# Kernel tuning notes

Measured on AMD Instinct MI355X. Metric: run time of the kernel, lower is better.

The kernel has to match this reference:

```python
import jax, jax.numpy as jnp
import numpy as np

QMAX = 127.0  # int8 symmetric quantization, num_bits=8
H, D, MRP = 16, 64, 32
DM = H * D  # d_model = 1024


def act_quant(x):
    # per-tensor symmetric int8 quant; returns quantized values (float-held) and scale
    scale = jnp.max(jnp.abs(x)) / QMAX + 1e-8
    y = x / scale
    q = jnp.clip(jnp.round(y), -QMAX, QMAX)
    return q, scale


def quant_linear(x, w, b):
    # TPUGEMMLinear: quantize activations and kernel per-tensor, int8 GEMM, dequant, add bias
    xq, sx = act_quant(x)
    wq, sw = act_quant(w)
    return jnp.matmul(xq, wq) * (sx * sw) + b


def setup_inputs() -> dict:
    key = jax.random.key(0)
    ks = jax.random.split(key, 8)
    B, Sq, Skv = 4, 1024, 1024
    inputs_q = jax.random.normal(ks[0], (B, Sq, DM), dtype=jnp.float32)
    inputs_kv = jax.random.normal(ks[1], (B, Skv, DM), dtype=jnp.float32)
    init_scale = 1.0 / np.sqrt(DM)  # lecun_normal-like
    Wq = jax.random.normal(ks[2], (DM, H * D), dtype=jnp.float32) * init_scale
    Wk = jax.random.normal(ks[3], (DM, H * D), dtype=jnp.float32) * init_scale
    Wv = jax.random.normal(ks[4], (DM, H * D), dtype=jnp.float32) * init_scale
    Wo = jax.random.normal(ks[5], (H * D, DM), dtype=jnp.float32) * init_scale
    bq = jnp.zeros((H * D,), jnp.float32)
    bk = jnp.zeros((H * D,), jnp.float32)
    bv = jnp.zeros((H * D,), jnp.float32)
    bo = jnp.zeros((DM,), jnp.float32)
    rel_pos_emb = jax.random.normal(ks[6], (2 * MRP + 1, D), dtype=jnp.float32) * 0.02
    return {"inputs_q": inputs_q, "inputs_kv": inputs_kv, "Wq": Wq, "bq": bq,
            "Wk": Wk, "bk": bk, "Wv": Wv, "bv": bv, "Wo": Wo, "bo": bo,
            "rel_pos_emb": rel_pos_emb}


def reference(inputs_q, inputs_kv, Wq, bq, Wk, bk, Wv, bv, Wo, bo, rel_pos_emb):
    B, Sq, _ = inputs_q.shape
    Skv = inputs_kv.shape[1]
    # quantized QKV projections
    q = quant_linear(inputs_q, Wq, bq).reshape(B, Sq, H, D).transpose(0, 2, 1, 3)   # [B,H,Sq,D]
    k = quant_linear(inputs_kv, Wk, bk).reshape(B, Skv, H, D).transpose(0, 2, 1, 3)  # [B,H,Skv,D]
    v = quant_linear(inputs_kv, Wv, bv).reshape(B, Skv, H, D).transpose(0, 2, 1, 3)  # [B,H,Skv,D]
    # relative position bias: gather emb rows per (q,k) offset -> [1,D?,Sq,Skv]
    positions = jnp.clip(jnp.arange(Sq)[:, None] - jnp.arange(Skv)[None, :] + MRP, 0, 2 * MRP)
    rel_pos_bias = rel_pos_emb[positions]                 # [Sq,Skv,D]
    rel_pos_bias = rel_pos_bias.transpose(2, 0, 1)[None]  # [1,D,Sq,Skv]; D==head_dim broadcasts over heads when D==H pattern; here added to [B,H,Sq,Skv] via broadcast of first H rows? No: faithful to original -> added directly
    # quantized QK^T
    kq, sk = act_quant(k.transpose(0, 1, 3, 2))  # [B,H,D,Skv]
    qq, sq = act_quant(q)
    content_scores = jnp.einsum('bhqd,bhdk->bhqk', qq, kq) * (sq * sk)
    attention_scores = content_scores + rel_pos_bias[:, :H]  # original broadcast-add of [1,D,Sq,Skv]; D>=H here (D=64,H=16) so slice matches broadcast semantics only when D==H; we take leading H planes to keep shapes consistent
    scale_factor = jnp.sqrt(jnp.float32(D)) * jnp.power(jnp.float32(min(Sq, Skv)), 0.25)
    attention_scores = attention_scores / scale_factor
    # manual stable softmax with +1e-6 in denominator (as in source)
    max_score = jnp.max(attention_scores, axis=-1, keepdims=True)
    exp_weights = jnp.exp(attention_scores - max_score)
    attention_weights = exp_weights / (jnp.sum(exp_weights, axis=-1, keepdims=True) + 1e-6)
    # quantized AV (weights unquantized, scale 1; values int8)
    vq, sv = act_quant(v)
    attention_output = jnp.einsum('bhqk,bhkd->bhqd', attention_weights, vq) * sv
    attention_output = attention_output.transpose(0, 2, 1, 3).reshape(B, Sq, H * D)
    return quant_linear(attention_output, Wo, bo)
```

## Files before the change

### kernel.cpp

```cpp
#include <hip/hip_runtime.h>
#include <hip/hip_bf16.h>
#include <stdint.h>

static constexpr int B_ = 4, S_ = 1024, H_ = 16, D_ = 64, DM_ = 1024;
static constexpr float SF_ = 45.254833221435546875f;
static constexpr float RCP_SF_ = 1.0f / SF_;
static constexpr float KC_ = (float)(1.4426950408889634074 / 45.254833221435546875);

typedef unsigned short u16;
typedef __attribute__((ext_vector_type(8))) short bf16x8;
typedef __attribute__((ext_vector_type(4))) float f32x4;

#define MFMA_BF16 __builtin_amdgcn_mfma_f32_16x16x32_bf16

typedef const __attribute__((address_space(1))) void CGV;
typedef __attribute__((address_space(3))) void LDSV;
__device__ __forceinline__ void gload16(const void* g, void* l) {
  __builtin_amdgcn_global_load_lds((CGV*)g, (LDSV*)l, 16, 0, 0);
}

__device__ __forceinline__ float slot_scale(const unsigned* s) {
  return __uint_as_float(*s) / 127.0f + 1e-8f;
}
__device__ __forceinline__ float quantf(float x, float s) {
  return fminf(fmaxf(rintf(x / s), -127.f), 127.f);
}
__device__ __forceinline__ u16 f2b(float x) {
  union { __hip_bfloat16 h; u16 u; } cv;
  cv.h = __float2bfloat16(x);
  return cv.u;
}
__device__ __forceinline__ float b2f(u16 u) { return __uint_as_float((unsigned)u << 16); }
__device__ __forceinline__ u16 qb16(float x, float s) { return f2b(quantf(x, s)); }

__global__ void zero_slots_kernel(unsigned* slots) {
  if (threadIdx.x < 16) slots[threadIdx.x] = 0u;
}

struct Ptr6 { const float* p[6]; int n4[6]; };

__global__ __launch_bounds__(256) void absmax6_kernel(Ptr6 a, unsigned* __restrict__ slots) {
  const int y = blockIdx.y;
  const float4* x4 = (const float4*)a.p[y];
  const int n4 = a.n4[y];
  float m = 0.f;
  for (int i = blockIdx.x * 256 + threadIdx.x; i < n4; i += gridDim.x * 256) {
    float4 v = x4[i];
    m = fmaxf(m, fmaxf(fmaxf(fabsf(v.x), fabsf(v.y)), fmaxf(fabsf(v.z), fabsf(v.w))));
  }
#pragma unroll
  for (int off = 32; off; off >>= 1) m = fmaxf(m, __shfl_xor(m, off));
  if ((threadIdx.x & 63) == 0) atomicMax(slots + y, __float_as_uint(m));
}

__device__ __forceinline__ void quant_body(const float* __restrict__ x, int n8, float s,
                                           u16* __restrict__ out) {
  for (int i = blockIdx.x * 256 + threadIdx.x; i < n8; i += gridDim.x * 256) {
    float4 v0 = *((const float4*)x + 2 * (size_t)i);
    float4 v1 = *((const float4*)x + 2 * (size_t)i + 1);
    int4 o;
    o.x = (int)qb16(v0.x, s) | ((int)qb16(v0.y, s) << 16);
    o.y = (int)qb16(v0.z, s) | ((int)qb16(v0.w, s) << 16);
    o.z = (int)qb16(v1.x, s) | ((int)qb16(v1.y, s) << 16);
    o.w = (int)qb16(v1.z, s) | ((int)qb16(v1.w, s) << 16);
    *((int4*)out + i) = o;
  }
}

__global__ __launch_bounds__(256) void quantize_bf16_kernel(const float* __restrict__ x, int n8,
                                                            const unsigned* __restrict__ slot,
                                                            u16* __restrict__ out) {
  quant_body(x, n8, slot_scale(slot), out);
}

__global__ __launch_bounds__(256) void quantize2_kernel(const float* __restrict__ x0,
                                                        const float* __restrict__ x1,
                                                        u16* __restrict__ o0, u16* __restrict__ o1,
                                                        const unsigned* __restrict__ slots, int n8) {
  const int y = blockIdx.y;
  quant_body(y ? x1 : x0, n8, slot_scale(slots + y), y ? o1 : o0);
}

struct QP3 { const float* tf[3]; };
__global__ __launch_bounds__(256) void quantP3_kernel(QP3 a, const unsigned* __restrict__ slots,
                                                      u16* __restrict__ q_p, u16* __restrict__ k_p,
                                                      u16* __restrict__ vT) {
  __shared__ u16 t[64][72];
  const int z = blockIdx.z;
  const float s = slot_scale(slots + 6 + z);
  const int tid = threadIdx.x;
  if (z < 2) {
    const float* xf = a.tf[z];
    u16* xp = z ? k_p : q_p;
    const int st = blockIdx.x & 15, bh = blockIdx.x >> 4;
    const int b = bh >> 4, h = bh & 15;
    const int r = tid >> 2, seg = (tid & 3) * 16;
    const float* src = &xf[((size_t)(b * S_) + st * 64 + r) * DM_ + h * 64 + seg];
    u16 qv[16];
#pragma unroll
    for (int i = 0; i < 16; i += 4) {
      float4 v = *(const float4*)(src + i);
      qv[i] = qb16(v.x, s); qv[i + 1] = qb16(v.y, s);
      qv[i + 2] = qb16(v.z, s); qv[i + 3] = qb16(v.w, s);
    }
    u16* dst = &xp[((size_t)bh * S_ + st * 64 + r) * 64 + seg];
    *(int4*)dst = *(const int4*)&qv[0];
    *(int4*)(dst + 8) = *(const int4*)&qv[8];
  } else {
    const float* vf = a.tf[2];
    const int h = blockIdx.x >> 6, bt = blockIdx.x & 63;
    const int b = bt >> 4, kt = bt & 15;
    const int row = tid >> 2, seg = (tid & 3) * 16;
    const float* src = &vf[((size_t)(b * S_) + kt * 64 + row) * DM_ + h * 64 + seg];
    float4 v0 = *(const float4*)src;
    float4 v1 = *(const float4*)(src + 4);
    float4 v2 = *(const float4*)(src + 8);
    float4 v3 = *(const float4*)(src + 12);
    t[seg + 0][row] = qb16(v0.x, s);  t[seg + 1][row] = qb16(v0.y, s);
    t[seg + 2][row] = qb16(v0.z, s);  t[seg + 3][row] = qb16(v0.w, s);
    t[seg + 4][row] = qb16(v1.x, s);  t[seg + 5][row] = qb16(v1.y, s);
    t[seg + 6][row] = qb16(v1.z, s);  t[seg + 7][row] = qb16(v1.w, s);
    t[seg + 8][row] = qb16(v2.x, s);  t[seg + 9][row] = qb16(v2.y, s);
    t[seg + 10][row] = qb16(v2.z, s); t[seg + 11][row] = qb16(v2.w, s);
    t[seg + 12][row] = qb16(v3.x, s); t[seg + 13][row] = qb16(v3.y, s);
    t[seg + 14][row] = qb16(v3.z, s); t[seg + 15][row] = qb16(v3.w, s);
    __syncthreads();
    const int d = tid >> 2, s2 = (tid & 3) * 16;
    u16* dst = &vT[((size_t)(b * 16 + h) * 64 + d) * (size_t)S_ + kt * 64 + s2];
    *(int4*)dst = *(const int4*)&t[d][s2];
    *(int4*)(dst + 8) = *(const int4*)&t[d][s2 + 8];
  }
}

struct W4 { const float* w[4]; u16* wt[4]; };
__global__ __launch_bounds__(256) void quantW4_kernel(W4 a, const unsigned* __restrict__ slots) {
  __shared__ u16 t[64][72];
  const int z = blockIdx.z;
  const float* w = a.w[z];
  u16* wt = a.wt[z];
  const float s = slot_scale(slots + 2 + z);
  const int k0 = blockIdx.y * 64, n0 = blockIdx.x * 64;
  const int tid = threadIdx.x;
#pragma unroll
  for (int rr = 0; rr < 4; rr++) {
    const int row = (tid >> 4) + rr * 16;
    const int col = (tid & 15) * 4;
    float4 v = *(const float4*)&w[(size_t)(k0 + row) * DM_ + n0 + col];
    t[col + 0][row] = qb16(v.x, s);
    t[col + 1][row] = qb16(v.y, s);
    t[col + 2][row] = qb16(v.z, s);
    t[col + 3][row] = qb16(v.w, s);
  }
  __syncthreads();
  const int nr = tid >> 2, kc = (tid & 3) * 16;
  *(int4*)&wt[(size_t)(n0 + nr) * DM_ + k0 + kc] = *(const int4*)&t[nr][kc];
  *(int4*)&wt[(size_t)(n0 + nr) * DM_ + k0 + kc + 8] = *(const int4*)&t[nr][kc + 8];
}

__device__ __forceinline__ void gemm_body(
    const u16* __restrict__ A, const u16* __restrict__ Bt,
    const unsigned* __restrict__ slotA, const unsigned* __restrict__ slotB,
    const float* __restrict__ bias, float* __restrict__ C,
    unsigned* __restrict__ amax_out,
    u16 (*As)[128][64], u16 (*Bs)[64][64]) {
  const int N = DM_, K = DM_;
  const int id = blockIdx.x;
  const int lin = (id & 7) * 64 + (id >> 3);
  const int by = lin >> 4, bx = lin & 15;
  const int m0 = by * 128, n0 = bx * 64;
  const int tid = threadIdx.x, w = tid >> 6, lane = tid & 63;
  const int c = lane & 15, g = lane >> 4;
  const int wr = w >> 1, wc = w & 1;
  const int lr = lane >> 3, lc = lane & 7;
  const int schunk = (lc ^ lr) << 3;

  f32x4 acc[4][2] = {};

  auto stage = [&](int buf, int kc) {
#pragma unroll
    for (int p = 0; p < 4; ++p) {
      const int r0 = w * 32 + p * 8;
      gload16(&A[(size_t)(m0 + r0 + lr) * K + kc + schunk], &As[buf][r0][0]);
    }
#pragma unroll
    for (int p = 0; p < 2; ++p) {
      const int r0 = w * 16 + p * 8;
      gload16(&Bt[(size_t)(n0 + r0 + lr) * K + kc + schunk], &Bs[buf][r0][0]);
    }
  };

  stage(0, 0);
  __syncthreads();
  for (int kt = 0; kt < 16; ++kt) {
    const int buf = kt & 1;
    if (kt < 15) stage(buf ^ 1, (kt + 1) * 64);
#pragma unroll
    for (int ks = 0; ks < 2; ++ks) {
      const int rswz = ((ks * 4 + g) ^ (c & 7)) << 3;
      bf16x8 b0 = *(const bf16x8*)&Bs[buf][wc * 32 + c][rswz];
      bf16x8 b1 = *(const bf16x8*)&Bs[buf][wc * 32 + 16 + c][rswz];
#pragma unroll
      for (int i = 0; i < 4; ++i) {
        bf16x8 av = *(const bf16x8*)&As[buf][wr * 64 + i * 16 + c][rswz];
        acc[i][0] = MFMA_BF16(av, b0, acc[i][0], 0, 0, 0);
        acc[i][1] = MFMA_BF16(av, b1, acc[i][1], 0, 0, 0);
      }
    }
    __syncthreads();
  }

  const float sAB = slot_scale(slotA) * slot_scale(slotB);
  float am = 0.f;
#pragma unroll
  for (int i = 0; i < 4; ++i)
#pragma unroll
    for (int j = 0; j < 2; ++j)
#pragma unroll
      for (int reg = 0; reg < 4; ++reg) {
        const int m = m0 + wr * 64 + i * 16 + 4 * g + reg;
        const int nn = n0 + wc * 32 + j * 16 + c;
        const float val = __fadd_rn(__fmul_rn(acc[i][j][reg], sAB), bias[nn]);
        C[(size_t)m * N + nn] = val;
        am = fmaxf(am, fabsf(val));
      }
  if (amax_out) {
#pragma unroll
    for (int off = 32; off; off >>= 1) am = fmaxf(am, __shfl_xor(am, off));
    if (lane == 0) atomicMax(amax_out, __float_as_uint(am));
  }
}

__global__ __launch_bounds__(256) void gemm128_kernel(
    const u16* __restrict__ A, const u16* __restrict__ Bt,
    const unsigned* __restrict__ slotA, const unsigned* __restrict__ slotB,
    const float* __restrict__ bias, float* __restrict__ C,
    unsigned* __restrict__ amax_out) {
  __shared__ u16 As[2][128][64];
  __shared__ u16 Bs[2][64][64];
  gemm_body(A, Bt, slotA, slotB, bias, C, amax_out, As, Bs);
}

struct G3 {
  const u16* A[3]; const u16* Bt[3]; const float* bias[3]; float* C[3];
};
__global__ __launch_bounds__(256) void gemm3_kernel(G3 a, unsigned* __restrict__ slots) {
  __shared__ u16 As[2][128][64];
  __shared__ u16 Bs[2][64][64];
  const int z = blockIdx.y;
  const unsigned* slotA = slots + (z == 0 ? 0 : 1);
  const unsigned* slotB = slots + 2 + z;
  gemm_body(a.A[z], a.Bt[z], slotA, slotB, a.bias[z], a.C[z], slots + 6 + z, As, Bs);
}

__global__ __launch_bounds__(256) void attn_kernel(
    const u16* __restrict__ qp_, const u16* __restrict__ kp_, const u16* __restrict__ vTb_,
    const unsigned* __restrict__ slots, const float* __restrict__ rel,
    float* __restrict__ ao, unsigned* __restrict__ amax_out) {
  __shared__ u16 Ks[2][64][64];
  __shared__ u16 Vs[2][64][64];
  __shared__ float Pf[4][16][68];
  __shared__ float biasT[68];
  __shared__ float Mrow[4][2][16];
  __shared__ float Frow[4][2][16];
  __shared__ float Lrow[4][2][16];

  const int id = blockIdx.x;
  const int rX = id & 7, rest = id >> 3;
  const int qoct = rest & 7, bhi = rest >> 3;
  const int gbh = rX * 8 + bhi;
  const int h = gbh & 15, b = gbh >> 4;

  const int tid = threadIdx.x;
  const int w = tid >> 6, lane = tid & 63;
  const int c = lane & 15, g = lane >> 4;
  const int lr = lane >> 3, lc = lane & 7;
  const int schunk = (lc ^ lr) << 3;

  const float sqk = slot_scale(slots + 6) * slot_scale(slots + 7);
  const float sv = slot_scale(slots + 8);
  if (tid < 65) biasT[tid] = rel[tid * D_ + h];

  const size_t ppan = (size_t)gbh * S_ * 64;
  const size_t vpan = (size_t)gbh * 64 * (size_t)S_;

  const int qb2[2] = {qoct * 128 + w * 16, qoct * 128 + 64 + w * 16};
  bf16x8 qA0[2], qA1[2];
#pragma unroll
  for (int u = 0; u < 2; ++u) {
    const size_t qrow = ppan + (size_t)(qb2[u] + c) * 64;
    qA0[u] = *(const bf16x8*)&qp_[qrow + g * 8];
    qA1[u] = *(const bf16x8*)&qp_[qrow + 32 + g * 8];
  }

  int4 kreg[2], vreg[2];
  auto loadK = [&](int ch) {
#pragma unroll
    for (int p = 0; p < 2; ++p)
      kreg[p] = *(const int4*)&kp_[ppan + (size_t)(ch * 64 + w * 16 + p * 8 + lr) * 64 + schunk];
  };
  auto writeK = [&](int buf) {
#pragma unroll
    for (int p = 0; p < 2; ++p)
      *(int4*)&Ks[buf][w * 16 + p * 8 + lr][lc * 8] = kreg[p];
  };
  auto loadV = [&](int ch) {
#pragma unroll
    for (int p = 0; p < 2; ++p)
      vreg[p] = *(const int4*)&vTb_[vpan + (size_t)(w * 16 + p * 8 + lr) * S_ + ch * 64 + schunk];
  };
  auto writeV = [&](int buf) {
#pragma unroll
    for (int p = 0; p < 2; ++p)
      *(int4*)&Vs[buf][w * 16 + p * 8 + lr][lc * 8] = vreg[p];
  };

  float M2[2][4], m2k[2][4], lsc[2] = {0.f, 0.f};
  f32x4 oacc[2][4] = {};
#pragma unroll
  for (int u = 0; u < 2; ++u)
#pragma unroll
    for (int reg = 0; reg < 4; ++reg) {
      M2[u][reg] = -3.4e38f;
      m2k[u][reg] = -3.4e38f * KC_;
    }

  loadK(0);
  loadV(0);
  writeK(0);
  writeV(0);
  __syncthreads();
  const float b_lo = biasT[0], b_hi = biasT[64];

  for (int ch = 0; ch < 16; ++ch) {
    const int buf = ch & 1;
    if (ch < 15) { loadK(ch + 1); loadV(ch + 1); }
#pragma unroll
    for (int u = 0; u < 2; ++u) {
      const int qbase = qb2[u];
      float mloc[4] = {-3.4e38f, -3.4e38f, -3.4e38f, -3.4e38f};
#pragma unroll
      for (int t = 0; t < 4; ++t) {
        f32x4 sacc = {0.f, 0.f, 0.f, 0.f};
        const int kr = t * 16 + c, sw = c & 7;
        bf16x8 k0 = *(const bf16x8*)&Ks[buf][kr][(g ^ sw) << 3];
        bf16x8 k1 = *(const bf16x8*)&Ks[buf][kr][((4 + g) ^ sw) << 3];
        sacc = MFMA_BF16(qA0[u], k0, sacc, 0, 0, 0);
        sacc = MFMA_BF16(qA1[u], k1, sacc, 0, 0, 0);
        const int kv0 = ch * 64 + t * 16;
        float bb[4];
        if (kv0 >= qbase + 47) {
          bb[0] = bb[1] = bb[2] = bb[3] = b_lo;
        } else if (qbase >= kv0 + 47) {
          bb[0] = bb[1] = bb[2] = bb[3] = b_hi;
        } else {
          const int jg = kv0 + c;
#pragma unroll
          for (int reg = 0; reg < 4; ++reg) {
            int dp = qbase + 4 * g + reg - jg + 32;
            dp = dp < 0 ? 0 : (dp > 64 ? 64 : dp);
            bb[reg] = biasT[dp];
          }
        }
        float* pw = &Pf[w][4 * g][t * 16 + c];
#pragma unroll
        for (int reg = 0; reg < 4; ++reg) {
          const float t2 = __fadd_rn(__fmul_rn(sacc[reg], sqk), bb[reg]);
          pw[reg * 68] = t2;
          mloc[reg] = fmaxf(mloc[reg], t2);
        }
      }
#pragma unroll
      for (int off = 1; off <= 8; off <<= 1)
#pragma unroll
        for (int reg = 0; reg < 4; ++reg)
          mloc[reg] = fmaxf(mloc[reg], __shfl_xor(mloc[reg], off));
      float f[4];
#pragma unroll
      for (int reg = 0; reg < 4; ++reg) {
        M2[u][reg] = fmaxf(M2[u][reg], mloc[reg]);
        const float mk = M2[u][reg] * KC_;
        f[reg] = exp2f(m2k[u][reg] - mk);
        m2k[u][reg] = mk;
      }
#pragma unroll
      for (int n = 0; n < 4; ++n)
#pragma unroll
        for (int reg = 0; reg < 4; ++reg) oacc[u][n][reg] *= f[reg];
      if (c < 4) {
        Mrow[w][u][4 * g + c] = m2k[u][c];
        Frow[w][u][4 * g + c] = f[c];
      }
      const float mkc = Mrow[w][u][c];
      lsc[u] = lsc[u] * Frow[w][u][c];
      float lacc = 0.f;
#pragma unroll
      for (int ks = 0; ks < 2; ++ks) {
        const float* pr = &Pf[w][c][ks * 32 + g * 8];
        float4 e0 = *(const float4*)pr;
        float4 e1 = *(const float4*)(pr + 4);
        float tv[8] = {e0.x, e0.y, e0.z, e0.w, e1.x, e1.y, e1.z, e1.w};
        bf16x8 ph, pm;
#pragma unroll
        for (int jj = 0; jj < 8; ++jj) {
          const float e = exp2f(fmaf(tv[jj], KC_, -mkc));
          lacc += e;
          const u16 hu = f2b(e);
          const float r1 = __fsub_rn(e, b2f(hu));
          const u16 mu = f2b(r1);
          ph[jj] = (short)hu;
          pm[jj] = (short)mu;
        }
#pragma unroll
        for (int n = 0; n < 4; ++n) {
          const int dd = 16 * n + c;
          bf16x8 vv = *(const bf16x8*)&Vs[buf][dd][((ks * 4 + g) ^ (c & 7)) << 3];
          oacc[u][n] = MFMA_BF16(ph, vv, oacc[u][n], 0, 0, 0);
          oacc[u][n] = MFMA_BF16(pm, vv, oacc[u][n], 0, 0, 0);
        }
      }
      lsc[u] += lacc;
    }
    if (ch < 15) { writeK(buf ^ 1); writeV(buf ^ 1); }
    __syncthreads();
  }

#pragma unroll
  for (int u = 0; u < 2; ++u) {
    float t = lsc[u];
    t += __shfl_xor(t, 16);
    t += __shfl_xor(t, 32);
    if (g == 0) Lrow[w][u][c] = t;
  }

  float am = 0.f;
#pragma unroll
  for (int u = 0; u < 2; ++u) {
#pragma unroll
    for (int reg = 0; reg < 4; ++reg) {
      const float L = Lrow[w][u][4 * g + reg] + 1e-6f;
      const size_t orow = ((size_t)(b * S_) + qb2[u] + 4 * g + reg) * DM_ + h * 64;
#pragma unroll
      for (int n = 0; n < 4; ++n) {
        const float val = __fmul_rn(oacc[u][n][reg] / L, sv);
        ao[orow + n * 16 + c] = val;
        am = fmaxf(am, fabsf(val));
      }
    }
  }
#pragma unroll
  for (int off = 1; off <= 32; off <<= 1) am = fmaxf(am, __shfl_xor(am, off));
  if (lane == 0) atomicMax(amax_out, __float_as_uint(am));
}

extern "C" void kernel_launch(void* const* d_in, const int* in_sizes, int n_in,
                              void* d_out, int out_size, void* d_ws, size_t ws_size,
                              hipStream_t stream) {
  const float* inputs_q  = (const float*)d_in[0];
  const float* inputs_kv = (const float*)d_in[1];
  const float* Wq = (const float*)d_in[2];
  const float* bq = (const float*)d_in[3];
  const float* Wk = (const float*)d_in[4];
  const float* bk = (const float*)d_in[5];
  const float* Wv = (const float*)d_in[6];
  const float* bv = (const float*)d_in[7];
  const float* Wo = (const float*)d_in[8];
  const float* bo = (const float*)d_in[9];
  const float* rel = (const float*)d_in[10];
  float* out = (float*)d_out;

  char* ws = (char*)d_ws;
  constexpr size_t MB = 1024 * 1024;
  unsigned* slots = (unsigned*)ws;
  u16* xq_b  = (u16*)(ws + 1024);
  u16* xkv_b = (u16*)((char*)xq_b + 8 * MB);
  u16* wq_b  = (u16*)((char*)xkv_b + 8 * MB);
  u16* wk_b  = (u16*)((char*)wq_b + 2 * MB);
  u16* wv_b  = (u16*)((char*)wk_b + 2 * MB);
  u16* wo_b  = (u16*)((char*)wv_b + 2 * MB);
  u16* q_p   = (u16*)((char*)wo_b + 2 * MB);
  u16* k_p   = (u16*)((char*)q_p + 8 * MB);
  u16* vT_b  = (u16*)((char*)k_p + 8 * MB);
  u16* ao_b  = (u16*)((char*)vT_b + 8 * MB);
  float* tf0 = (float*)((char*)ao_b + 8 * MB);
  float* tf1 = (float*)((char*)tf0 + 16 * MB);
  float* tf2 = (float*)((char*)tf1 + 16 * MB);
  float* aof = tf0;
  (void)ws_size; (void)in_sizes; (void)n_in; (void)out_size;

  const int n4_x = (B_ * S_ * DM_) / 4, n4_w = (DM_ * DM_) / 4;
  const int n8_x = (B_ * S_ * DM_) / 8;

  zero_slots_kernel<<<1, 64, 0, stream>>>(slots);

  Ptr6 a6;
  a6.p[0] = inputs_q;  a6.n4[0] = n4_x;
  a6.p[1] = inputs_kv; a6.n4[1] = n4_x;
  a6.p[2] = Wq; a6.n4[2] = n4_w;
  a6.p[3] = Wk; a6.n4[3] = n4_w;
  a6.p[4] = Wv; a6.n4[4] = n4_w;
  a6.p[5] = Wo; a6.n4[5] = n4_w;
  absmax6_kernel<<<dim3(128, 6), 256, 0, stream>>>(a6, slots);

  quantize2_kernel<<<dim3(512, 2), 256, 0, stream>>>(inputs_q, inputs_kv, xq_b, xkv_b,
                                                     slots, n8_x);
  W4 w4;
  w4.w[0] = Wq; w4.wt[0] = wq_b;
  w4.w[1] = Wk; w4.wt[1] = wk_b;
  w4.w[2] = Wv; w4.wt[2] = wv_b;
  w4.w[3] = Wo; w4.wt[3] = wo_b;
  quantW4_kernel<<<dim3(16, 16, 4), 256, 0, stream>>>(w4, slots);

  G3 g3;
  g3.A[0] = xq_b;  g3.Bt[0] = wq_b; g3.bias[0] = bq; g3.C[0] = tf0;
  g3.A[1] = xkv_b; g3.Bt[1] = wk_b; g3.bias[1] = bk; g3.C[1] = tf1;
  g3.A[2] = xkv_b; g3.Bt[2] = wv_b; g3.bias[2] = bv; g3.C[2] = tf2;
  gemm3_kernel<<<dim3(512, 3), 256, 0, stream>>>(g3, slots);

  QP3 qp3;
  qp3.tf[0] = tf0; qp3.tf[1] = tf1; qp3.tf[2] = tf2;
  quantP3_kernel<<<dim3(1024, 1, 3), 256, 0, stream>>>(qp3, slots, q_p, k_p, vT_b);

  attn_kernel<<<512, 256, 0, stream>>>(q_p, k_p, vT_b, slots, rel, aof, slots + 9);

  quantize_bf16_kernel<<<1024, 256, 0, stream>>>(aof, n8_x, slots + 9, ao_b);

  gemm128_kernel<<<512, 256, 0, stream>>>(ao_b, wo_b, slots + 9, slots + 5, bo, out, nullptr);
}
```

Measured before the change: 306.6 us.

## Widen QKV GEMM tile to 128x128 and merge input/weight quantize kernels

The fused QKV projection GEMM now uses 128x128 output tiles with a 4x4 MFMA accumulator per wave, up from 128x64. This halves the block count and raises operand reuse per LDS load, at the cost of more registers and LDS per block. The separate input-quantize and weight-quantize/transpose kernels are merged into one launch indexed by blockIdx.z to save one launch. Weight slices leave their surplus blocks idle.

```diff
diff --git a/kernel.cpp b/kernel.cpp
--- a/kernel.cpp
+++ b/kernel.cpp
@@ -73,12 +73,39 @@
   quant_body(x, n8, slot_scale(slot), out);
 }
 
-__global__ __launch_bounds__(256) void quantize2_kernel(const float* __restrict__ x0,
-                                                        const float* __restrict__ x1,
-                                                        u16* __restrict__ o0, u16* __restrict__ o1,
-                                                        const unsigned* __restrict__ slots, int n8) {
-  const int y = blockIdx.y;
-  quant_body(y ? x1 : x0, n8, slot_scale(slots + y), y ? o1 : o0);
+struct QIW {
+  const float* xq; const float* xkv; u16* xqo; u16* xkvo;
+  const float* w[4]; u16* wt[4];
+};
+__global__ __launch_bounds__(256) void quantIW_kernel(QIW a, const unsigned* __restrict__ slots,
+                                                      int n8) {
+  __shared__ u16 t[64][72];
+  const int z = blockIdx.z;
+  const int tid = threadIdx.x;
+  if (z < 2) {
+    quant_body(z ? a.xkv : a.xq, n8, slot_scale(slots + z), z ? a.xkvo : a.xqo);
+  } else {
+    if (blockIdx.x >= 256) return;
+    const int zz = z - 2;
+    const float* w = a.w[zz];
+    u16* wt = a.wt[zz];
+    const float s = slot_scale(slots + 2 + zz);
+    const int k0 = (blockIdx.x >> 4) * 64, n0 = (blockIdx.x & 15) * 64;
+#pragma unroll
+    for (int rr = 0; rr < 4; rr++) {
+      const int row = (tid >> 4) + rr * 16;
+      const int col = (tid & 15) * 4;
+      float4 v = *(const float4*)&w[(size_t)(k0 + row) * DM_ + n0 + col];
+      t[col + 0][row] = qb16(v.x, s);
+      t[col + 1][row] = qb16(v.y, s);
+      t[col + 2][row] = qb16(v.z, s);
+      t[col + 3][row] = qb16(v.w, s);
+    }
+    __syncthreads();
+    const int nr = tid >> 2, kc = (tid & 3) * 16;
+    *(int4*)&wt[(size_t)(n0 + nr) * DM_ + k0 + kc] = *(const int4*)&t[nr][kc];
+    *(int4*)&wt[(size_t)(n0 + nr) * DM_ + k0 + kc + 8] = *(const int4*)&t[nr][kc + 8];
+  }
 }
 
 struct QP3 { const float* tf[3]; };
@@ -132,37 +159,13 @@
   }
 }
 
-struct W4 { const float* w[4]; u16* wt[4]; };
-__global__ __launch_bounds__(256) void quantW4_kernel(W4 a, const unsigned* __restrict__ slots) {
-  __shared__ u16 t[64][72];
-  const int z = blockIdx.z;
-  const float* w = a.w[z];
-  u16* wt = a.wt[z];
-  const float s = slot_scale(slots + 2 + z);
-  const int k0 = blockIdx.y * 64, n0 = blockIdx.x * 64;
-  const int tid = threadIdx.x;
-#pragma unroll
-  for (int rr = 0; rr < 4; rr++) {
-    const int row = (tid >> 4) + rr * 16;
-    const int col = (tid & 15) * 4;
-    float4 v = *(const float4*)&w[(size_t)(k0 + row) * DM_ + n0 + col];
-    t[col + 0][row] = qb16(v.x, s);
-    t[col + 1][row] = qb16(v.y, s);
-    t[col + 2][row] = qb16(v.z, s);
-    t[col + 3][row] = qb16(v.w, s);
-  }
-  __syncthreads();
-  const int nr = tid >> 2, kc = (tid & 3) * 16;
-  *(int4*)&wt[(size_t)(n0 + nr) * DM_ + k0 + kc] = *(const int4*)&t[nr][kc];
-  *(int4*)&wt[(size_t)(n0 + nr) * DM_ + k0 + kc + 8] = *(const int4*)&t[nr][kc + 8];
-}
-
-__device__ __forceinline__ void gemm_body(
+__global__ __launch_bounds__(256) void gemm128_kernel(
     const u16* __restrict__ A, const u16* __restrict__ Bt,
     const unsigned* __restrict__ slotA, const unsigned* __restrict__ slotB,
     const float* __restrict__ bias, float* __restrict__ C,
-    unsigned* __restrict__ amax_out,
-    u16 (*As)[128][64], u16 (*Bs)[64][64]) {
+    unsigned* __restrict__ amax_out) {
+  __shared__ u16 As[2][128][64];
+  __shared__ u16 Bs[2][64][64];
   const int N = DM_, K = DM_;
   const int id = blockIdx.x;
   const int lin = (id & 7) * 64 + (id >> 3);
@@ -230,26 +233,83 @@
   }
 }
 
-__global__ __launch_bounds__(256) void gemm128_kernel(
-    const u16* __restrict__ A, const u16* __restrict__ Bt,
-    const unsigned* __restrict__ slotA, const unsigned* __restrict__ slotB,
-    const float* __restrict__ bias, float* __restrict__ C,
-    unsigned* __restrict__ amax_out) {
-  __shared__ u16 As[2][128][64];
-  __shared__ u16 Bs[2][64][64];
-  gemm_body(A, Bt, slotA, slotB, bias, C, amax_out, As, Bs);
-}
-
 struct G3 {
   const u16* A[3]; const u16* Bt[3]; const float* bias[3]; float* C[3];
 };
 __global__ __launch_bounds__(256) void gemm3_kernel(G3 a, unsigned* __restrict__ slots) {
   __shared__ u16 As[2][128][64];
-  __shared__ u16 Bs[2][64][64];
+  __shared__ u16 Bs[2][128][64];
   const int z = blockIdx.y;
+  const u16* __restrict__ A = a.A[z];
+  const u16* __restrict__ Bt = a.Bt[z];
+  const float* __restrict__ bias = a.bias[z];
+  float* __restrict__ C = a.C[z];
   const unsigned* slotA = slots + (z == 0 ? 0 : 1);
   const unsigned* slotB = slots + 2 + z;
-  gemm_body(a.A[z], a.Bt[z], slotA, slotB, a.bias[z], a.C[z], slots + 6 + z, As, Bs);
+  unsigned* amax_out = slots + 6 + z;
+
+  const int N = DM_, K = DM_;
+  const int id = blockIdx.x;
+  const int lin = (id & 7) * 32 + (id >> 3);
+  const int by = lin >> 3, bx = lin & 7;
+  const int m0 = by * 128, n0 = bx * 128;
+  const int tid = threadIdx.x, w = tid >> 6, lane = tid & 63;
+  const int c = lane & 15, g = lane >> 4;
+  const int wr = w >> 1, wc = w & 1;
+  const int lr = lane >> 3, lc = lane & 7;
+  const int schunk = (lc ^ lr) << 3;
+
+  f32x4 acc[4][4] = {};
+
+  auto stage = [&](int buf, int kc) {
+#pragma unroll
+    for (int p = 0; p < 4; ++p) {
+      const int r0 = w * 32 + p * 8;
+      gload16(&A[(size_t)(m0 + r0 + lr) * K + kc + schunk], &As[buf][r0][0]);
+      gload16(&Bt[(size_t)(n0 + r0 + lr) * K + kc + schunk], &Bs[buf][r0][0]);
+    }
+  };
+
+  stage(0, 0);
+  __syncthreads();
+  for (int kt = 0; kt < 16; ++kt) {
+    const int buf = kt & 1;
+    if (kt < 15) stage(buf ^ 1, (kt + 1) * 64);
+#pragma unroll
+    for (int ks = 0; ks < 2; ++ks) {
+      const int rswz = ((ks * 4 + g) ^ (c & 7)) << 3;
+      bf16x8 bv[4];
+#pragma unroll
+      for (int j = 0; j < 4; ++j)
+        bv[j] = *(const bf16x8*)&Bs[buf][wc * 64 + j * 16 + c][rswz];
+#pragma unroll
+      for (int i = 0; i < 4; ++i) {
+        bf16x8 av = *(const bf16x8*)&As[buf][wr * 64 + i * 16 + c][rswz];
+#pragma unroll
+        for (int j = 0; j < 4; ++j)
+          acc[i][j] = MFMA_BF16(av, bv[j], acc[i][j], 0, 0, 0);
+      }
+    }
+    __syncthreads();
+  }
+
+  const float sAB = slot_scale(slotA) * slot_scale(slotB);
+  float am = 0.f;
+#pragma unroll
+  for (int i = 0; i < 4; ++i)
+#pragma unroll
+    for (int j = 0; j < 4; ++j)
+#pragma unroll
+      for (int reg = 0; reg < 4; ++reg) {
+        const int m = m0 + wr * 64 + i * 16 + 4 * g + reg;
+        const int nn = n0 + wc * 64 + j * 16 + c;
+        const float val = __fadd_rn(__fmul_rn(acc[i][j][reg], sAB), bias[nn]);
+        C[(size_t)m * N + nn] = val;
+        am = fmaxf(am, fabsf(val));
+      }
+#pragma unroll
+  for (int off = 32; off; off >>= 1) am = fmaxf(am, __shfl_xor(am, off));
+  if (lane == 0) atomicMax(amax_out, __float_as_uint(am));
 }
 
 __global__ __launch_bounds__(256) void attn_kernel(
@@ -501,20 +561,19 @@
   a6.p[5] = Wo; a6.n4[5] = n4_w;
   absmax6_kernel<<<dim3(128, 6), 256, 0, stream>>>(a6, slots);
 
-  quantize2_kernel<<<dim3(512, 2), 256, 0, stream>>>(inputs_q, inputs_kv, xq_b, xkv_b,
-                                                     slots, n8_x);
-  W4 w4;
-  w4.w[0] = Wq; w4.wt[0] = wq_b;
-  w4.w[1] = Wk; w4.wt[1] = wk_b;
-  w4.w[2] = Wv; w4.wt[2] = wv_b;
-  w4.w[3] = Wo; w4.wt[3] = wo_b;
-  quantW4_kernel<<<dim3(16, 16, 4), 256, 0, stream>>>(w4, slots);
+  QIW qiw;
+  qiw.xq = inputs_q; qiw.xkv = inputs_kv; qiw.xqo = xq_b; qiw.xkvo = xkv_b;
+  qiw.w[0] = Wq; qiw.wt[0] = wq_b;
+  qiw.w[1] = Wk; qiw.wt[1] = wk_b;
+  qiw.w[2] = Wv; qiw.wt[2] = wv_b;
+  qiw.w[3] = Wo; qiw.wt[3] = wo_b;
+  quantIW_kernel<<<dim3(512, 1, 6), 256, 0, stream>>>(qiw, slots, n8_x);
 
   G3 g3;
   g3.A[0] = xq_b;  g3.Bt[0] = wq_b; g3.bias[0] = bq; g3.C[0] = tf0;
   g3.A[1] = xkv_b; g3.Bt[1] = wk_b; g3.bias[1] = bk; g3.C[1] = tf1;
   g3.A[2] = xkv_b; g3.Bt[2] = wv_b; g3.bias[2] = bv; g3.C[2] = tf2;
-  gemm3_kernel<<<dim3(512, 3), 256, 0, stream>>>(g3, slots);
+  gemm3_kernel<<<dim3(256, 3), 256, 0, stream>>>(g3, slots);
 
   QP3 qp3;
   qp3.tf[0] = tf0; qp3.tf[1] = tf1; qp3.tf[2] = tf2;
```

Result: faster. 284.1 us (-7.3%).
